# Kernel tuning notes

Measured on AMD Instinct MI355X. Metric: run time of the kernel, lower is better.

## Reference

```python
import jax, jax.numpy as jnp
import numpy as np

B, C, D, H, W = 1, 32, 48, 64, 208
EPS = 1e-5  # BatchNorm eps


def setup_inputs() -> dict:
    key = jax.random.key(0)
    ks = jax.random.split(key, 8)
    x = jax.random.normal(ks[0], (B, C, D, H, W), jnp.float32)
    g = jax.random.normal(ks[1], (B, 20, H, W), jnp.float32)
    conv_w = jax.random.normal(ks[2], (C, C, 3, 3, 3), jnp.float32) * 0.02
    bn1_gamma = 1.0 + 0.1 * jax.random.normal(ks[3], (C,), jnp.float32)
    bn1_beta = 0.1 * jax.random.normal(ks[4], (C,), jnp.float32)
    bn1_mean = 0.1 * jax.random.normal(ks[5], (C,), jnp.float32)
    bn1_var = jax.random.uniform(ks[6], (C,), jnp.float32, 0.5, 1.5)
    bn2_gamma = 1.0 + 0.1 * jax.random.normal(ks[7], (C,), jnp.float32)
    bn2_beta = jnp.zeros((C,), jnp.float32)
    bn2_mean = jnp.zeros((C,), jnp.float32)
    bn2_var = jnp.ones((C,), jnp.float32)
    return {
        'x': x, 'g': g, 'conv_w': conv_w,
        'bn1_gamma': bn1_gamma, 'bn1_beta': bn1_beta, 'bn1_mean': bn1_mean, 'bn1_var': bn1_var,
        'bn2_gamma': bn2_gamma, 'bn2_beta': bn2_beta, 'bn2_mean': bn2_mean, 'bn2_var': bn2_var,
    }


def _l1_normalize(k):
    # F.normalize(k, p=1, dim=1)
    return k / jnp.maximum(jnp.sum(jnp.abs(k), axis=1, keepdims=True), 1e-12)


def _sga_scan(x, w):
    """Directional semi-global aggregation along the LAST axis.
    x: [B,C,D,H,L] cost volume, w: [B,5,H,L] L1-normalized guidance weights.
    Recurrence (GANet SGA):
      A[p,d] = w0*x[p,d] + w1*A[p-1,d] + w2*A[p-1,d-1] + w3*A[p-1,d+1] + w4*max_d' A[p-1,d']
    """
    xs = jnp.moveaxis(x, -1, 0)  # [L,B,C,D,H]
    ws = jnp.moveaxis(w, -1, 0)  # [L,B,5,H]

    def step(prev, inp):
        xi, wi = inp  # [B,C,D,H], [B,5,H]
        w0, w1, w2, w3, w4 = [wi[:, i][:, None, None, :] for i in range(5)]
        up = jnp.concatenate([prev[:, :, :1], prev[:, :, :-1]], axis=2)   # A[d-1]
        dn = jnp.concatenate([prev[:, :, 1:], prev[:, :, -1:]], axis=2)   # A[d+1]
        mx = jnp.max(prev, axis=2, keepdims=True)                          # max_d A
        out = w0 * xi + w1 * prev + w2 * up + w3 * dn + w4 * mx
        return out, out

    _, outs = jax.lax.scan(step, xs[0], (xs, ws))  # boundary: carry init = raw cost slice
    return jnp.moveaxis(outs, 0, -1)


def _sga(x, k1, k2, k3, k4):
    # direction 1: left -> right (along W)
    d1 = _sga_scan(x, k1)
    # direction 2: right -> left
    d2 = jnp.flip(_sga_scan(jnp.flip(x, -1), jnp.flip(k2, -1)), -1)
    # vertical directions: swap H<->W so the scan axis is H
    xv = jnp.swapaxes(x, 3, 4)  # [B,C,D,W,H]
    d3 = jnp.swapaxes(_sga_scan(xv, jnp.swapaxes(k3, 2, 3)), 3, 4)  # top -> bottom
    d4 = jnp.swapaxes(
        jnp.flip(_sga_scan(jnp.flip(xv, -1), jnp.flip(jnp.swapaxes(k4, 2, 3), -1)), -1), 3, 4)
    # GANet combines directions with an elementwise max
    return jnp.maximum(jnp.maximum(d1, d2), jnp.maximum(d3, d4))


def _bn3d(x, gamma, beta, mean, var):
    s = (gamma / jnp.sqrt(var + EPS))[None, :, None, None, None]
    return (x - mean[None, :, None, None, None]) * s + beta[None, :, None, None, None]


def _conv3d_same(x, w):
    return jax.lax.conv_general_dilated(
        x, w, window_strides=(1, 1, 1), padding=[(1, 1)] * 3,
        dimension_numbers=('NCDHW', 'OIDHW', 'NCDHW'))


def reference(x, g, conv_w, bn1_gamma, bn1_beta, bn1_mean, bn1_var,
              bn2_gamma, bn2_beta, bn2_mean, bn2_var):
    rem = x
    k1, k2, k3, k4 = jnp.split(g, 4, axis=1)  # each [B,5,H,W]
    k1, k2, k3, k4 = map(_l1_normalize, (k1, k2, k3, k4))
    a = _sga(x, k1, k2, k3, k4)
    # refine=True branch: BN+ReLU then BasicConv(3x3x3, BN, no relu)
    a = jax.nn.relu(_bn3d(a, bn1_gamma, bn1_beta, bn1_mean, bn1_var))
    a = _conv3d_same(a, conv_w)
    a = _bn3d(a, bn2_gamma, bn2_beta, bn2_mean, bn2_var)
    return jax.nn.relu(a + rem)
```

## Files before the change

### kernel.cpp

```cpp
#include <hip/hip_runtime.h>
#include <hip/hip_bf16.h>
#include <cstddef>

#define C_ 32
#define D_ 48
#define DP_ 50
#define H_ 64
#define W_ 208
#define WP_ 210
#define HW_ 13312
#define HS_ 9984
#define EPS_ 1e-5f

typedef __attribute__((ext_vector_type(8))) short short8;
typedef __attribute__((ext_vector_type(4))) float float4v;
typedef __attribute__((ext_vector_type(16))) float float16v;
typedef __attribute__((ext_vector_type(2))) __fp16 half2v;

template<int CTRL>
__device__ __forceinline__ float dppmov(float x) {
    int v = __builtin_bit_cast(int, x);
    return __builtin_bit_cast(float,
        __builtin_amdgcn_update_dpp(v, v, CTRL, 0xf, 0xf, false));
}
template<int CTRL>
__device__ __forceinline__ float dppmax(float m) {
    return fmaxf(m, dppmov<CTRL>(m));
}
__device__ __forceinline__ float rl(float v, int idx) {
    return __builtin_bit_cast(float,
        __builtin_amdgcn_readlane(__builtin_bit_cast(int, v), idx));
}
template<int CTRL>
__device__ __forceinline__ unsigned dppu(unsigned x) {
    return (unsigned)__builtin_amdgcn_update_dpp((int)x, (int)x, CTRL, 0xf, 0xf, false);
}
__device__ __forceinline__ unsigned rlu(unsigned v, int idx) {
    return (unsigned)__builtin_amdgcn_readlane((int)v, idx);
}
__device__ __forceinline__ unsigned pkmax_u(unsigned a, unsigned b) {
    unsigned r;
    asm("v_pk_max_f16 %0, %1, %2" : "=v"(r) : "v"(a), "v"(b));
    return r;
}
__device__ __forceinline__ half2v hcast(unsigned u) { return __builtin_bit_cast(half2v, u); }
__device__ __forceinline__ unsigned ucast(half2v h) { return __builtin_bit_cast(unsigned, h); }

__device__ __forceinline__ float sga_step_dpp(float A, float xi,
    float w0, float w1, float w2, float w3, float w4, bool actv, bool ge47)
{
    float up = dppmov<0x138>(A);
    float dn = dppmov<0x130>(A);
    dn = ge47 ? A : dn;
    float m = actv ? A : -3.4e38f;
    m = dppmax<0x111>(m);
    m = dppmax<0x112>(m);
    m = dppmax<0x114>(m);
    m = dppmax<0x118>(m);
    m = dppmax<0x142>(m);
    m = dppmax<0x143>(m);
    float mall = rl(m, 63);
    return (w0*xi + w1*A) + ((w2*up + w3*dn) + w4*mall);
}

__device__ __forceinline__ unsigned sga_step_pk(unsigned Au, unsigned xiu,
    unsigned w0, unsigned w1, unsigned w2, unsigned w3, unsigned w4,
    bool actv, bool ge47)
{
    unsigned up = dppu<0x138>(Au);
    unsigned dn = dppu<0x130>(Au);
    dn = ge47 ? Au : dn;
    unsigned m = actv ? Au : 0xFBFFFBFFu;
    m = pkmax_u(m, dppu<0x111>(m));
    m = pkmax_u(m, dppu<0x112>(m));
    m = pkmax_u(m, dppu<0x114>(m));
    m = pkmax_u(m, dppu<0x118>(m));
    m = pkmax_u(m, dppu<0x142>(m));
    m = pkmax_u(m, dppu<0x143>(m));
    unsigned mall = rlu(m, 63);
    half2v A = hcast(Au), xi = hcast(xiu), uph = hcast(up), dnh = hcast(dn),
           mh = hcast(mall), h0 = hcast(w0), h1 = hcast(w1), h2 = hcast(w2),
           h3 = hcast(w3), h4 = hcast(w4);
    half2v r = (h0 * xi + h1 * A) + ((h2 * uph + h3 * dnh) + h4 * mh);
    return ucast(r);
}

__global__ __launch_bounds__(256) void prep_kernel(
    const float* __restrict__ g, const float* __restrict__ cw,
    float* __restrict__ wn, float* __restrict__ wnT,
    __hip_bfloat16* __restrict__ wrep, unsigned* __restrict__ actu)
{
    int idx = blockIdx.x * 256 + threadIdx.x;
    if (idx < 4 * HW_) {
        int dir = idx / HW_;
        int hw  = idx % HW_;
        const float* gb = g + dir * 5 * HW_ + hw;
        float v0 = gb[0*HW_], v1 = gb[1*HW_], v2 = gb[2*HW_], v3 = gb[3*HW_], v4 = gb[4*HW_];
        float s = fabsf(v0)+fabsf(v1)+fabsf(v2)+fabsf(v3)+fabsf(v4);
        float inv = 1.0f / fmaxf(s, 1e-12f);
        v0 *= inv; v1 *= inv; v2 *= inv; v3 *= inv; v4 *= inv;
        float* ob = wn + dir * 5 * HW_ + hw;
        ob[0*HW_] = v0; ob[1*HW_] = v1; ob[2*HW_] = v2; ob[3*HW_] = v3; ob[4*HW_] = v4;
        if (dir >= 2) {
            int hq = hw / W_, wq = hw % W_;
            float* oT = wnT + ((size_t)((dir-2)*5)*W_ + wq)*H_ + hq;
            oT[0]       = v0; oT[1*HW_] = v1; oT[2*HW_] = v2;
            oT[3*HW_]   = v3; oT[4*HW_] = v4;
        }
    } else if (idx < 4 * HW_ + 27648) {
        int j = idx - 4 * HW_;
        int e    = j & 7;
        int lane = (j >> 3) & 63;
        int q    = j >> 9;
        int cih  = q & 1;
        int tap  = q >> 1;
        int co = lane & 31;
        int ci = cih * 16 + (lane >> 5) * 8 + e;
        wrep[j] = __float2bfloat16(cw[(co * C_ + ci) * 27 + tap]);
    } else if (idx < 4 * HW_ + 27648 + 98304) {
        int j2 = idx - (4 * HW_ + 27648);
        int hd  = j2 >> 5;
        int r   = j2 & 31;
        int col = (r >> 4) ? 209 : 0;
        int cu  = r & 15;
        int h = hd / 48, dd = hd % 48;
        actu[(((size_t)h * DP_ + dd + 1) * WP_ + col) * 16 + cu] = 0u;
    } else {
        int j3 = idx - (4 * HW_ + 27648 + 98304);
        int pl   = j3 >= 215040;
        int r3   = pl ? j3 - 215040 : j3;
        int h    = r3 / 3360;
        int rest = r3 % 3360;
        int dpad = pl ? (DP_ - 1) : 0;
        actu[((size_t)h * DP_ + dpad) * WP_ * 16 + rest] = 0u;
    }
}

__global__ __launch_bounds__(256) void t0_kernel(
    const float* __restrict__ x, __hip_bfloat16* __restrict__ xt)
{
    __shared__ float t[48 * 257];
    int tid = threadIdx.x;
    int c  = blockIdx.x / 52;
    int q0 = (blockIdx.x % 52) * 256;
    #pragma unroll
    for (int dd = 0; dd < 48; ++dd)
        t[dd * 257 + tid] = x[((size_t)c * 48 + dd) * HW_ + q0 + tid];
    __syncthreads();
    unsigned* xtu = (unsigned*)xt;
    #pragma unroll
    for (int k = 0; k < 24; ++k) {
        int f = tid + 256 * k;
        int d2 = f % 24, hwl = f / 24;
        union { unsigned u; __hip_bfloat16 hh[2]; } pk;
        pk.hh[0] = __float2bfloat16(t[(2 * d2) * 257 + hwl]);
        pk.hh[1] = __float2bfloat16(t[(2 * d2 + 1) * 257 + hwl]);
        xtu[(((size_t)c * HW_ + q0 + hwl) * 48 + 2 * d2) >> 1] = pk.u;
    }
}

__global__ __launch_bounds__(256, 4) void sga_w_kernel(
    const __hip_bfloat16* __restrict__ xt, const float* __restrict__ wn,
    __hip_bfloat16* __restrict__ d12)
{
    __shared__ __fp16 sO[2][2][208][48];

    int lane = threadIdx.x & 63;
    int widb = threadIdx.x >> 6;
    int rowb = widb >> 1;
    int dir  = widb & 1;
    int grow = blockIdx.x * 2 + rowb;
    int c = grow >> 6, h = grow & 63;
    int d = lane < 48 ? lane : 47;
    bool actv = lane < 48, ge47 = lane >= 47;
    const __hip_bfloat16* xp = xt + ((size_t)c * HW_ + h * W_) * 48 + d;
    const float* wb = wn + (size_t)dir * 5 * HW_ + h * W_;
    int il = lane >> 3, jl = lane & 7;
    bool wact = il < 5;

    float xb[3][8];
    float wAr[3];

    if (dir == 0) {
        #pragma unroll
        for (int j = 0; j < 8; ++j) {
            xb[0][j] = __bfloat162float(xp[(size_t)j * 48]);
            xb[1][j] = __bfloat162float(xp[(size_t)(8 + j) * 48]);
        }
        wAr[0] = wact ? wb[il * HW_ + jl] : 0.0f;
        wAr[1] = wact ? wb[il * HW_ + 8 + jl] : 0.0f;
        float A = xb[0][0];
        #pragma unroll
        for (int cc = 0; cc < 26; ++cc) {
            const int buf = cc % 3;
            if (cc < 24) {
                const int nb = (cc + 2) % 3;
                #pragma unroll
                for (int j = 0; j < 8; ++j)
                    xb[nb][j] = __bfloat162float(xp[(size_t)((cc + 2) * 8 + j) * 48]);
                wAr[nb] = wact ? wb[il * HW_ + (cc + 2) * 8 + jl] : 0.0f;
            }
            #pragma unroll
            for (int j = 0; j < 8; ++j) {
                A = sga_step_dpp(A, xb[buf][j], rl(wAr[buf], j), rl(wAr[buf], 8 + j),
                                 rl(wAr[buf], 16 + j), rl(wAr[buf], 24 + j),
                                 rl(wAr[buf], 32 + j), actv, ge47);
                if (actv) sO[rowb][0][cc * 8 + j][d] = (__fp16)A;
            }
        }
    } else {
        #pragma unroll
        for (int j = 0; j < 8; ++j) {
            xb[0][j] = __bfloat162float(xp[(size_t)(200 + j) * 48]);
            xb[1][j] = __bfloat162float(xp[(size_t)(192 + j) * 48]);
        }
        wAr[0] = wact ? wb[il * HW_ + 200 + jl] : 0.0f;
        wAr[1] = wact ? wb[il * HW_ + 192 + jl] : 0.0f;
        float A = xb[0][7];
        #pragma unroll
        for (int cc2 = 0; cc2 < 26; ++cc2) {
            const int cc = 25 - cc2;
            const int buf = cc2 % 3;
            if (cc2 < 24) {
                const int nb = (cc2 + 2) % 3;
                #pragma unroll
                for (int j = 0; j < 8; ++j)
                    xb[nb][j] = __bfloat162float(xp[(size_t)((cc - 2) * 8 + j) * 48]);
                wAr[nb] = wact ? wb[il * HW_ + (cc - 2) * 8 + jl] : 0.0f;
            }
            #pragma unroll
            for (int j = 7; j >= 0; --j) {
                A = sga_step_dpp(A, xb[buf][j], rl(wAr[buf], j), rl(wAr[buf], 8 + j),
                                 rl(wAr[buf], 16 + j), rl(wAr[buf], 24 + j),
                                 rl(wAr[buf], 32 + j), actv, ge47);
                if (actv) sO[rowb][1][cc * 8 + j][d] = (__fp16)A;
            }
        }
    }

    __syncthreads();

    __hip_bfloat16* dp = d12 + ((size_t)c * HW_ + h * W_) * 48 + d;
    if (actv) {
        const int p0 = dir * 104;
        #pragma unroll
        for (int t = 0; t < 104; ++t) {
            int p = p0 + t;
            float d1 = (float)sO[rowb][0][p][d];
            float d2 = (float)sO[rowb][1][p][d];
            dp[(size_t)p * 48] = __float2bfloat16(fmaxf(d1, d2));
        }
    }
}

__global__ __launch_bounds__(128, 3) void sga_h_kernel(
    const __hip_bfloat16* __restrict__ xt, const float* __restrict__ wnT,
    __hip_bfloat16* __restrict__ d12,
    const float* __restrict__ g1, const float* __restrict__ b1,
    const float* __restrict__ m1, const float* __restrict__ v1)
{
    __shared__ unsigned sO[2][64][48];

    int lane = threadIdx.x & 63;
    int dir  = threadIdx.x >> 6;
    int gp   = blockIdx.x;
    int g0 = gp * 2;
    int c = g0 / W_, w = g0 % W_;
    int d = lane < 48 ? lane : 47;
    bool actv = lane < 48, ge47 = lane >= 47;
    const __hip_bfloat16* xA = xt + ((size_t)c * HW_ + w) * 48 + d;
    const __hip_bfloat16* xB = xA + 48;
    const float* wbA = wnT + ((size_t)(dir * 5) * W_ + w) * H_;
    const float* wbB = wbA + H_;
    int il = lane >> 3, jl = lane & 7;
    bool wact = il < 5;

    unsigned xpk[3][8];
    unsigned wAr[3];

    if (dir == 0) {
        #pragma unroll
        for (int b = 0; b < 2; ++b) {
            #pragma unroll
            for (int j = 0; j < 8; ++j) {
                float fA = __bfloat162float(xA[(size_t)(b * 8 + j) * HS_]);
                float fB = __bfloat162float(xB[(size_t)(b * 8 + j) * HS_]);
                xpk[b][j] = ucast(__builtin_amdgcn_cvt_pkrtz(fA, fB));
            }
            float wfA = wact ? wbA[il * HW_ + b * 8 + jl] : 0.0f;
            float wfB = wact ? wbB[il * HW_ + b * 8 + jl] : 0.0f;
            wAr[b] = ucast(__builtin_amdgcn_cvt_pkrtz(wfA, wfB));
        }
        unsigned Au = xpk[0][0];
        #pragma unroll
        for (int cc = 0; cc < 8; ++cc) {
            const int buf = cc % 3;
            if (cc < 6) {
                const int nb = (cc + 2) % 3;
                #pragma unroll
                for (int j = 0; j < 8; ++j) {
                    float fA = __bfloat162float(xA[(size_t)((cc + 2) * 8 + j) * HS_]);
                    float fB = __bfloat162float(xB[(size_t)((cc + 2) * 8 + j) * HS_]);
                    xpk[nb][j] = ucast(__builtin_amdgcn_cvt_pkrtz(fA, fB));
                }
                float wfA = wact ? wbA[il * HW_ + (cc + 2) * 8 + jl] : 0.0f;
                float wfB = wact ? wbB[il * HW_ + (cc + 2) * 8 + jl] : 0.0f;
                wAr[nb] = ucast(__builtin_amdgcn_cvt_pkrtz(wfA, wfB));
            }
            #pragma unroll
            for (int j = 0; j < 8; ++j) {
                Au = sga_step_pk(Au, xpk[buf][j], rlu(wAr[buf], j), rlu(wAr[buf], 8 + j),
                                 rlu(wAr[buf], 16 + j), rlu(wAr[buf], 24 + j),
                                 rlu(wAr[buf], 32 + j), actv, ge47);
                if (actv) sO[0][cc * 8 + j][d] = Au;
            }
        }
    } else {
        #pragma unroll
        for (int b = 0; b < 2; ++b) {
            const int base = 56 - b * 8;
            #pragma unroll
            for (int j = 0; j < 8; ++j) {
                float fA = __bfloat162float(xA[(size_t)(base + j) * HS_]);
                float fB = __bfloat162float(xB[(size_t)(base + j) * HS_]);
                xpk[b][j] = ucast(__builtin_amdgcn_cvt_pkrtz(fA, fB));
            }
            float wfA = wact ? wbA[il * HW_ + base + jl] : 0.0f;
            float wfB = wact ? wbB[il * HW_ + base + jl] : 0.0f;
            wAr[b] = ucast(__builtin_amdgcn_cvt_pkrtz(wfA, wfB));
        }
        unsigned Au = xpk[0][7];
        #pragma unroll
        for (int cc2 = 0; cc2 < 8; ++cc2) {
            const int cc = 7 - cc2;
            const int buf = cc2 % 3;
            if (cc2 < 6) {
                const int nb = (cc2 + 2) % 3;
                #pragma unroll
                for (int j = 0; j < 8; ++j) {
                    float fA = __bfloat162float(xA[(size_t)((cc - 2) * 8 + j) * HS_]);
                    float fB = __bfloat162float(xB[(size_t)((cc - 2) * 8 + j) * HS_]);
                    xpk[nb][j] = ucast(__builtin_amdgcn_cvt_pkrtz(fA, fB));
                }
                float wfA = wact ? wbA[il * HW_ + (cc - 2) * 8 + jl] : 0.0f;
                float wfB = wact ? wbB[il * HW_ + (cc - 2) * 8 + jl] : 0.0f;
                wAr[nb] = ucast(__builtin_amdgcn_cvt_pkrtz(wfA, wfB));
            }
            #pragma unroll
            for (int j = 7; j >= 0; --j) {
                Au = sga_step_pk(Au, xpk[buf][j], rlu(wAr[buf], j), rlu(wAr[buf], 8 + j),
                                 rlu(wAr[buf], 16 + j), rlu(wAr[buf], 24 + j),
                                 rlu(wAr[buf], 32 + j), actv, ge47);
                if (actv) sO[1][cc * 8 + j][d] = Au;
            }
        }
    }

    __syncthreads();

    float s1 = g1[c] * rsqrtf(v1[c] + EPS_);
    float o1 = b1[c] - m1[c] * s1;
    __hip_bfloat16* dpA = d12 + ((size_t)c * HW_ + w) * 48 + d;
    __hip_bfloat16* dpB = dpA + 48;
    #pragma unroll
    for (int t = 0; t < 32; ++t) {
        int h = dir * 32 + t;
        unsigned um = pkmax_u(sO[0][h][d], sO[1][h][d]);
        half2v mh = hcast(um);
        if (actv) {
            float vA = fmaxf((float)mh[0], __bfloat162float(dpA[(size_t)h * HS_]));
            float vB = fmaxf((float)mh[1], __bfloat162float(dpB[(size_t)h * HS_]));
            dpA[(size_t)h * HS_] = __float2bfloat16(fmaxf(vA * s1 + o1, 0.0f));
            dpB[(size_t)h * HS_] = __float2bfloat16(fmaxf(vB * s1 + o1, 0.0f));
        }
    }
}

__global__ __launch_bounds__(256) void trans_kernel(
    const __hip_bfloat16* __restrict__ st, __hip_bfloat16* __restrict__ act)
{
    __shared__ float t[8 * 1571];
    int tid = threadIdx.x;
    int h  = blockIdx.x / 26;
    int w0 = (blockIdx.x % 26) * 8;
    const unsigned* stu = (const unsigned*)st;
    #pragma unroll
    for (int k = 0; k < 24; ++k) {
        int f = tid + 256 * k;
        int d2 = f % 24, wl = (f / 24) % 8, c = f / 192;
        unsigned u = stu[(((size_t)c * HW_ + h * W_ + w0 + wl) * 48 + 2 * d2) >> 1];
        const __hip_bfloat16* bp = (const __hip_bfloat16*)&u;
        t[wl * 1571 + c * 49 + 2 * d2]     = __bfloat162float(bp[0]);
        t[wl * 1571 + c * 49 + 2 * d2 + 1] = __bfloat162float(bp[1]);
    }
    __syncthreads();
    unsigned* actu = (unsigned*)act;
    #pragma unroll
    for (int k = 0; k < 24; ++k) {
        int f = tid + 256 * k;
        int cp = f % 16, wl = (f / 16) % 8, d = f / 128;
        union { unsigned u; __hip_bfloat16 hh[2]; } pk;
        pk.hh[0] = __float2bfloat16(t[wl * 1571 + (2 * cp) * 49 + d]);
        pk.hh[1] = __float2bfloat16(t[wl * 1571 + (2 * cp + 1) * 49 + d]);
        actu[(((size_t)h * DP_ + d + 1) * WP_ + w0 + wl + 1) * 16 + cp] = pk.u;
    }
}

__global__ __launch_bounds__(256, 4) void conv_kernel(
    const __hip_bfloat16* __restrict__ act,
    const short8* __restrict__ wrep,
    const float* __restrict__ x,
    const float* __restrict__ g2, const float* __restrict__ b2,
    const float* __restrict__ m2, const float* __restrict__ v2,
    float* __restrict__ out)
{
    __shared__ __hip_bfloat16 sAct[10 * 34 * 40];

    int tid  = threadIdx.x;
    int lane = tid & 63;
    int v    = tid >> 6;
    int bid  = blockIdx.x;
    int wt   = bid % 7;
    int t    = bid / 7;
    int h    = t & 63;
    int d0b  = (t >> 6) * 8;
    int w0   = wt * 32;
    int n    = lane & 31;
    int half = lane >> 5;

    float16v acc0 = (float16v)(0.0f);
    float16v acc1 = (float16v)(0.0f);

    const short8* ap8 = (const short8*)act;

    #pragma unroll
    for (int kh = 0; kh < 3; ++kh) {
        int hh = h + kh - 1;
        if (hh < 0 || hh >= H_) continue;
        __syncthreads();
        #pragma unroll
        for (int k = 0; k < 6; ++k) {
            int i = tid + 256 * k;
            if (i < 1360) {
                int dp = i / 136;
                int r  = i - dp * 136;
                int wl = r >> 2, q = r & 3;
                int wc = w0 + wl; wc = wc < 209 ? wc : 209;
                short8 vd = ap8[(((size_t)hh * DP_ + d0b + dp) * WP_ + wc) * 4 + q];
                *(short8*)&sAct[(dp * 34 + wl) * 40 + q * 8] = vd;
            }
        }
        __syncthreads();
        #pragma unroll
        for (int kw = 0; kw < 3; ++kw) {
            #pragma unroll
            for (int cih = 0; cih < 2; ++cih) {
                short8 af[3];
                #pragma unroll
                for (int kd = 0; kd < 3; ++kd)
                    af[kd] = wrep[(((kd*3 + kh)*3 + kw)*2 + cih)*64 + lane];
                short8 bf[4];
                #pragma unroll
                for (int p = 0; p < 4; ++p)
                    bf[p] = *(const short8*)
                        &sAct[((2*v + p) * 34 + kw + n) * 40 + cih * 16 + half * 8];
                #pragma unroll
                for (int kd = 0; kd < 3; ++kd) {
                    acc0 = __builtin_amdgcn_mfma_f32_32x32x16_bf16(af[kd], bf[kd],   acc0, 0, 0, 0);
                    acc1 = __builtin_amdgcn_mfma_f32_32x32x16_bf16(af[kd], bf[kd+1], acc1, 0, 0, 0);
                }
            }
        }
    }

    int d0 = d0b + 2 * v;
    int wl = w0 + n;
    bool wvalid = wl < W_;
    int coh = 4 * half;
    #pragma unroll
    for (int r = 0; r < 16; ++r) {
        int co = (r & 3) + 8 * (r >> 2) + coh;
        float s2 = g2[co] * rsqrtf(v2[co] + EPS_);
        float o2 = b2[co] - m2[co] * s2;
        size_t idx0 = ((size_t)(co * D_ + d0) * H_ + h) * W_ + wl;
        if (wvalid) {
            out[idx0]       = fmaxf(acc0[r] * s2 + o2 + x[idx0],       0.0f);
            out[idx0 + HW_] = fmaxf(acc1[r] * s2 + o2 + x[idx0 + HW_], 0.0f);
        }
    }
}

extern "C" void kernel_launch(void* const* d_in, const int* in_sizes, int n_in,
                              void* d_out, int out_size, void* d_ws, size_t ws_size,
                              hipStream_t stream)
{
    const float* x    = (const float*)d_in[0];
    const float* g    = (const float*)d_in[1];
    const float* cw   = (const float*)d_in[2];
    const float* bn1g = (const float*)d_in[3];
    const float* bn1b = (const float*)d_in[4];
    const float* bn1m = (const float*)d_in[5];
    const float* bn1v = (const float*)d_in[6];
    const float* bn2g = (const float*)d_in[7];
    const float* bn2b = (const float*)d_in[8];
    const float* bn2m = (const float*)d_in[9];
    const float* bn2v = (const float*)d_in[10];
    float* out = (float*)d_out;

    char* ws = (char*)d_ws;
    float* wn  = (float*)ws;
    float* wnT = (float*)(ws + 1064960);
    __hip_bfloat16* wrep = (__hip_bfloat16*)(ws + 1597440);
    __hip_bfloat16* d12t = (__hip_bfloat16*)(ws + 1652736);
    __hip_bfloat16* act  = (__hip_bfloat16*)(ws + 42547200);
    __hip_bfloat16* xt = (__hip_bfloat16*)out;

    prep_kernel<<<2380, 256, 0, stream>>>(g, cw, wn, wnT, wrep, (unsigned*)act);
    t0_kernel<<<1664, 256, 0, stream>>>(x, xt);
    sga_w_kernel<<<1024, 256, 0, stream>>>(xt, wn, d12t);
    sga_h_kernel<<<3328, 128, 0, stream>>>(xt, wnT, d12t, bn1g, bn1b, bn1m, bn1v);
    trans_kernel<<<1664, 256, 0, stream>>>(d12t, act);
    conv_kernel<<<2688, 256, 0, stream>>>(act, (const short8*)wrep, x,
                                          bn2g, bn2b, bn2m, bn2v, out);
}
```

Before: 397.4 us.

## Pack two image rows into fp16x2 lanes for the horizontal SGA scan

The W-direction SGA kernel now processes two adjacent rows per wavefront by packing both rows' states into half2 registers and reusing the existing packed sga_step_pk routine. This halves the number of serial recurrence steps per row pair, which are bound by DPP and readlane latency. The forward-direction results are spilled to a scratch region in the output buffer instead of shared memory, which cuts LDS use but adds global memory traffic. Blocks shrink to 128 threads, and the recurrence now runs in fp16 rather than fp32, which lowers accuracy.

```diff
diff --git a/kernel.cpp b/kernel.cpp
--- a/kernel.cpp
+++ b/kernel.cpp
@@ -45,23 +45,6 @@
 }
 __device__ __forceinline__ half2v hcast(unsigned u) { return __builtin_bit_cast(half2v, u); }
 __device__ __forceinline__ unsigned ucast(half2v h) { return __builtin_bit_cast(unsigned, h); }
-
-__device__ __forceinline__ float sga_step_dpp(float A, float xi,
-    float w0, float w1, float w2, float w3, float w4, bool actv, bool ge47)
-{
-    float up = dppmov<0x138>(A);
-    float dn = dppmov<0x130>(A);
-    dn = ge47 ? A : dn;
-    float m = actv ? A : -3.4e38f;
-    m = dppmax<0x111>(m);
-    m = dppmax<0x112>(m);
-    m = dppmax<0x114>(m);
-    m = dppmax<0x118>(m);
-    m = dppmax<0x142>(m);
-    m = dppmax<0x143>(m);
-    float mall = rl(m, 63);
-    return (w0*xi + w1*A) + ((w2*up + w3*dn) + w4*mall);
-}
 
 __device__ __forceinline__ unsigned sga_step_pk(unsigned Au, unsigned xiu,
     unsigned w0, unsigned w1, unsigned w2, unsigned w3, unsigned w4,
@@ -159,64 +142,81 @@
     }
 }
 
-__global__ __launch_bounds__(256, 4) void sga_w_kernel(
+__global__ __launch_bounds__(128, 2) void sga_w_kernel(
     const __hip_bfloat16* __restrict__ xt, const float* __restrict__ wn,
-    __hip_bfloat16* __restrict__ d12)
-{
-    __shared__ __fp16 sO[2][2][208][48];
+    __hip_bfloat16* __restrict__ d12, unsigned* __restrict__ d1tmp)
+{
+    __shared__ unsigned sO[208][48];
 
     int lane = threadIdx.x & 63;
-    int widb = threadIdx.x >> 6;
-    int rowb = widb >> 1;
-    int dir  = widb & 1;
-    int grow = blockIdx.x * 2 + rowb;
-    int c = grow >> 6, h = grow & 63;
+    int dir  = threadIdx.x >> 6;
+    int pairI = blockIdx.x;
+    int c  = pairI >> 5;
+    int h0 = (pairI & 31) * 2;
     int d = lane < 48 ? lane : 47;
     bool actv = lane < 48, ge47 = lane >= 47;
-    const __hip_bfloat16* xp = xt + ((size_t)c * HW_ + h * W_) * 48 + d;
-    const float* wb = wn + (size_t)dir * 5 * HW_ + h * W_;
+    const __hip_bfloat16* xA = xt + ((size_t)c * HW_ + h0 * W_) * 48 + d;
+    const __hip_bfloat16* xB = xA + HS_;
+    const float* wbA = wn + (size_t)dir * 5 * HW_ + h0 * W_;
     int il = lane >> 3, jl = lane & 7;
     bool wact = il < 5;
-
-    float xb[3][8];
-    float wAr[3];
+    unsigned* tmpp = d1tmp + (size_t)pairI * 208 * 48 + d;
+
+    unsigned xpk[3][8];
+    unsigned wAr[3];
 
     if (dir == 0) {
         #pragma unroll
-        for (int j = 0; j < 8; ++j) {
-            xb[0][j] = __bfloat162float(xp[(size_t)j * 48]);
-            xb[1][j] = __bfloat162float(xp[(size_t)(8 + j) * 48]);
-        }
-        wAr[0] = wact ? wb[il * HW_ + jl] : 0.0f;
-        wAr[1] = wact ? wb[il * HW_ + 8 + jl] : 0.0f;
-        float A = xb[0][0];
+        for (int b = 0; b < 2; ++b) {
+            #pragma unroll
+            for (int j = 0; j < 8; ++j) {
+                float fA = __bfloat162float(xA[(size_t)(b * 8 + j) * 48]);
+                float fB = __bfloat162float(xB[(size_t)(b * 8 + j) * 48]);
+                xpk[b][j] = ucast(__builtin_amdgcn_cvt_pkrtz(fA, fB));
+            }
+            float wfA = wact ? wbA[il * HW_ + b * 8 + jl] : 0.0f;
+            float wfB = wact ? wbA[il * HW_ + W_ + b * 8 + jl] : 0.0f;
+            wAr[b] = ucast(__builtin_amdgcn_cvt_pkrtz(wfA, wfB));
+        }
+        unsigned Au = xpk[0][0];
         #pragma unroll
         for (int cc = 0; cc < 26; ++cc) {
             const int buf = cc % 3;
             if (cc < 24) {
                 const int nb = (cc + 2) % 3;
                 #pragma unroll
-                for (int j = 0; j < 8; ++j)
-                    xb[nb][j] = __bfloat162float(xp[(size_t)((cc + 2) * 8 + j) * 48]);
-                wAr[nb] = wact ? wb[il * HW_ + (cc + 2) * 8 + jl] : 0.0f;
+                for (int j = 0; j < 8; ++j) {
+                    float fA = __bfloat162float(xA[(size_t)((cc + 2) * 8 + j) * 48]);
+                    float fB = __bfloat162float(xB[(size_t)((cc + 2) * 8 + j) * 48]);
+                    xpk[nb][j] = ucast(__builtin_amdgcn_cvt_pkrtz(fA, fB));
+                }
+                float wfA = wact ? wbA[il * HW_ + (cc + 2) * 8 + jl] : 0.0f;
+                float wfB = wact ? wbA[il * HW_ + W_ + (cc + 2) * 8 + jl] : 0.0f;
+                wAr[nb] = ucast(__builtin_amdgcn_cvt_pkrtz(wfA, wfB));
             }
             #pragma unroll
             for (int j = 0; j < 8; ++j) {
-                A = sga_step_dpp(A, xb[buf][j], rl(wAr[buf], j), rl(wAr[buf], 8 + j),
-                                 rl(wAr[buf], 16 + j), rl(wAr[buf], 24 + j),
-                                 rl(wAr[buf], 32 + j), actv, ge47);
-                if (actv) sO[rowb][0][cc * 8 + j][d] = (__fp16)A;
+                Au = sga_step_pk(Au, xpk[buf][j], rlu(wAr[buf], j), rlu(wAr[buf], 8 + j),
+                                 rlu(wAr[buf], 16 + j), rlu(wAr[buf], 24 + j),
+                                 rlu(wAr[buf], 32 + j), actv, ge47);
+                if (actv) tmpp[(size_t)(cc * 8 + j) * 48] = Au;
             }
         }
     } else {
         #pragma unroll
-        for (int j = 0; j < 8; ++j) {
-            xb[0][j] = __bfloat162float(xp[(size_t)(200 + j) * 48]);
-            xb[1][j] = __bfloat162float(xp[(size_t)(192 + j) * 48]);
-        }
-        wAr[0] = wact ? wb[il * HW_ + 200 + jl] : 0.0f;
-        wAr[1] = wact ? wb[il * HW_ + 192 + jl] : 0.0f;
-        float A = xb[0][7];
+        for (int b = 0; b < 2; ++b) {
+            const int base = 200 - b * 8;
+            #pragma unroll
+            for (int j = 0; j < 8; ++j) {
+                float fA = __bfloat162float(xA[(size_t)(base + j) * 48]);
+                float fB = __bfloat162float(xB[(size_t)(base + j) * 48]);
+                xpk[b][j] = ucast(__builtin_amdgcn_cvt_pkrtz(fA, fB));
+            }
+            float wfA = wact ? wbA[il * HW_ + base + jl] : 0.0f;
+            float wfB = wact ? wbA[il * HW_ + W_ + base + jl] : 0.0f;
+            wAr[b] = ucast(__builtin_amdgcn_cvt_pkrtz(wfA, wfB));
+        }
+        unsigned Au = xpk[0][7];
         #pragma unroll
         for (int cc2 = 0; cc2 < 26; ++cc2) {
             const int cc = 25 - cc2;
@@ -224,31 +224,38 @@
             if (cc2 < 24) {
                 const int nb = (cc2 + 2) % 3;
                 #pragma unroll
-                for (int j = 0; j < 8; ++j)
-                    xb[nb][j] = __bfloat162float(xp[(size_t)((cc - 2) * 8 + j) * 48]);
-                wAr[nb] = wact ? wb[il * HW_ + (cc - 2) * 8 + jl] : 0.0f;
+                for (int j = 0; j < 8; ++j) {
+                    float fA = __bfloat162float(xA[(size_t)((cc - 2) * 8 + j) * 48]);
+                    float fB = __bfloat162float(xB[(size_t)((cc - 2) * 8 + j) * 48]);
+                    xpk[nb][j] = ucast(__builtin_amdgcn_cvt_pkrtz(fA, fB));
+                }
+                float wfA = wact ? wbA[il * HW_ + (cc - 2) * 8 + jl] : 0.0f;
+                float wfB = wact ? wbA[il * HW_ + W_ + (cc - 2) * 8 + jl] : 0.0f;
+                wAr[nb] = ucast(__builtin_amdgcn_cvt_pkrtz(wfA, wfB));
             }
             #pragma unroll
             for (int j = 7; j >= 0; --j) {
-                A = sga_step_dpp(A, xb[buf][j], rl(wAr[buf], j), rl(wAr[buf], 8 + j),
-                                 rl(wAr[buf], 16 + j), rl(wAr[buf], 24 + j),
-                                 rl(wAr[buf], 32 + j), actv, ge47);
-                if (actv) sO[rowb][1][cc * 8 + j][d] = (__fp16)A;
+                Au = sga_step_pk(Au, xpk[buf][j], rlu(wAr[buf], j), rlu(wAr[buf], 8 + j),
+                                 rlu(wAr[buf], 16 + j), rlu(wAr[buf], 24 + j),
+                                 rlu(wAr[buf], 32 + j), actv, ge47);
+                if (actv) sO[cc * 8 + j][d] = Au;
             }
         }
     }
 
     __syncthreads();
 
-    __hip_bfloat16* dp = d12 + ((size_t)c * HW_ + h * W_) * 48 + d;
+    __hip_bfloat16* dpA = d12 + ((size_t)c * HW_ + h0 * W_) * 48 + d;
+    __hip_bfloat16* dpB = dpA + HS_;
     if (actv) {
         const int p0 = dir * 104;
-        #pragma unroll
+        #pragma unroll 8
         for (int t = 0; t < 104; ++t) {
             int p = p0 + t;
-            float d1 = (float)sO[rowb][0][p][d];
-            float d2 = (float)sO[rowb][1][p][d];
-            dp[(size_t)p * 48] = __float2bfloat16(fmaxf(d1, d2));
+            unsigned um = pkmax_u(tmpp[(size_t)p * 48], sO[p][d]);
+            half2v mh = hcast(um);
+            dpA[(size_t)p * 48] = __float2bfloat16((float)mh[0]);
+            dpB[(size_t)p * 48] = __float2bfloat16((float)mh[1]);
         }
     }
 }
@@ -514,10 +521,11 @@
     __hip_bfloat16* d12t = (__hip_bfloat16*)(ws + 1652736);
     __hip_bfloat16* act  = (__hip_bfloat16*)(ws + 42547200);
     __hip_bfloat16* xt = (__hip_bfloat16*)out;
+    unsigned* d1tmp = (unsigned*)((char*)out + 40894464);
 
     prep_kernel<<<2380, 256, 0, stream>>>(g, cw, wn, wnT, wrep, (unsigned*)act);
     t0_kernel<<<1664, 256, 0, stream>>>(x, xt);
-    sga_w_kernel<<<1024, 256, 0, stream>>>(xt, wn, d12t);
+    sga_w_kernel<<<1024, 128, 0, stream>>>(xt, wn, d12t, d1tmp);
     sga_h_kernel<<<3328, 128, 0, stream>>>(xt, wnT, d12t, bn1g, bn1b, bn1m, bn1v);
     trans_kernel<<<1664, 256, 0, stream>>>(d12t, act);
     conv_kernel<<<2688, 256, 0, stream>>>(act, (const short8*)wrep, x,
```

After: 382.8 us. 3.7% less time.
